# Performance work log

Measured on AMD Instinct MI355X. Metric: run time of the kernel, lower is better.

Reference implementation:

```python
import jax, jax.numpy as jnp
import numpy as np

HEADDIM = 32
BLOCK = 256


def segsum(x):
    """Stable segment sum. x: (..., T) -> (..., T, T) with -inf above diagonal."""
    T = x.shape[-1]
    xe = jnp.broadcast_to(x[..., :, None], x.shape + (T,))  # (..., T, T)
    lower_strict = jnp.tril(jnp.ones((T, T), dtype=bool), -1)
    xe = jnp.where(lower_strict, xe, 0.0)
    x_segsum = jnp.cumsum(xe, axis=-2)
    lower = jnp.tril(jnp.ones((T, T), dtype=bool), 0)
    return jnp.where(lower, x_segsum, -jnp.inf)


def ssd_chunked(X, A, B, C, block_len):
    """Chunked SSD (Mamba2) scan, L assumed divisible by block_len.
    X: (b,L,h,p)  A: (b,L,h)  B,C: (b,L,h,n). Returns Y: (b,L,h,p)."""
    b, L, h, p = X.shape
    c = L // block_len
    X = X.reshape(b, c, block_len, h, p)
    A = A.reshape(b, c, block_len, h).transpose(0, 3, 1, 2)  # b h c l
    B = B.reshape(b, c, block_len, h, -1)
    C = C.reshape(b, c, block_len, h, -1)

    A_cumsum = jnp.cumsum(A, axis=-1)                         # b h c l
    Lmat = jnp.exp(segsum(A))                                 # b h c l s
    Y_diag = jnp.einsum('bclhn,bcshn,bhcls,bcshp->bclhp', C, B, Lmat, X)

    decay_states = jnp.exp(A_cumsum[:, :, :, -1:] - A_cumsum)  # b h c l
    states = jnp.einsum('bclhn,bhcl,bclhp->bchpn', B, decay_states, X)
    init = jnp.zeros_like(states[:, :1])
    states = jnp.concatenate([init, states], axis=1)           # b (c+1) h p n

    chunk_sums = jnp.pad(A_cumsum[:, :, :, -1], ((0, 0), (0, 0), (1, 0)))  # b h (c+1)
    decay_chunk = jnp.exp(segsum(chunk_sums))                  # b h (c+1) (c+1)
    new_states = jnp.einsum('bhzc,bchpn->bzhpn', decay_chunk, states)
    inter_states = new_states[:, :-1]                          # b c h p n

    state_decay_out = jnp.exp(A_cumsum)                        # b h c l
    Y_off = jnp.einsum('bclhn,bchpn,bhcl->bclhp', C, inter_states, state_decay_out)
    return (Y_diag + Y_off).reshape(b, L, h, p)


def setup_inputs() -> dict:
    key = jax.random.key(0)
    k1, k2, k3 = jax.random.split(key, 3)
    Bsz, L, D = 2, 4096, 1024
    hidden_states = jax.random.normal(k1, (Bsz, L, D), dtype=jnp.float32)
    boundary_prob = jax.random.uniform(k2, (Bsz, L), minval=0.01, maxval=0.99, dtype=jnp.float32)
    boundary_mask = jax.random.uniform(k3, (Bsz, L)) < 0.25
    boundary_mask = boundary_mask.at[:, 0].set(True)  # first token must be a boundary
    return {"hidden_states": hidden_states, "boundary_prob": boundary_prob,
            "boundary_mask": boundary_mask}


def reference(hidden_states, boundary_prob, boundary_mask):
    Bsz, L, D = hidden_states.shape
    nheads = D // HEADDIM

    # --- Chunk layer: stable gather of boundary tokens to the front (M = L) ---
    token_idx = jnp.arange(L)[None, :] + (~boundary_mask).astype(jnp.int32) * L
    order = jnp.argsort(token_idx, axis=1)                    # (B, L)
    h = jnp.take_along_axis(hidden_states, order[:, :, None], axis=1)
    p = jnp.take_along_axis(boundary_prob, order, axis=1)

    # --- DeChunk: EMA reconstruction via chunked SSD scan ---
    p = jnp.clip(p, 1e-4, 1.0 - 1e-4)
    dt = jnp.log(1.0 / (1.0 - p))                              # (B, L)
    x = (h / dt[..., None]).reshape(Bsz, L, nheads, HEADDIM)
    X = x * dt[..., None, None]                                # = h, scaled form used by SSD
    A_seq = jnp.broadcast_to(-dt[..., None], (Bsz, L, nheads))  # A = -1 per head
    Bm = jnp.broadcast_to(p[..., None, None], (Bsz, L, nheads, 1))
    Cm = jnp.ones_like(Bm)
    Y = ssd_chunked(X, A_seq, Bm, Cm, BLOCK)                   # (B, L, h, p)
    out = Y.reshape(Bsz, L, D)

    # --- Plug back: each original position reads latest boundary's EMA value ---
    idx = jnp.clip(jnp.cumsum(boundary_mask.astype(jnp.int32), axis=1) - 1, 0, L - 1)
    return jnp.take_along_axis(out, idx[:, :, None], axis=1)
```

## Files before the change

kernel.cpp:

```cpp
#include <hip/hip_runtime.h>
#include <hip/hip_bf16.h>

#define SEQL 4096
#define DIM  1024
#define TR   16
#define LOOKBACK 128
#define WCAP 32
#define DSCUT -8.0f

typedef float f32x4 __attribute__((ext_vector_type(4)));

__global__ __launch_bounds__(256) void solo_kernel(
    const float* __restrict__ h, const float* __restrict__ prob,
    const int* __restrict__ mask, float* __restrict__ out) {
  const int bx  = blockIdx.x;
  const int s   = (bx & 7) * (SEQL / TR / 8) + (bx >> 3);
  const int t0  = s * TR;
  const int b   = blockIdx.y;
  const int tid = threadIdx.x, wid = tid >> 6, lane = tid & 63;
  const int tok = t0 - LOOKBACK + tid;

  __shared__ float lw[WCAP];
  __shared__ int   lp[WCAP];
  __shared__ float inb_b[TR];
  __shared__ int   wsC[4];
  __shared__ float wsS[4];

  int mv = 0; float pv = 0.f, la = 0.f;
  if (tid < LOOKBACK + TR && tok >= 0) {
    mv = (mask[b * SEQL + tok] != 0);
    float p = prob[b * SEQL + tok];
    pv = fminf(fmaxf(p, 1e-4f), 1.f - 1e-4f);
    la = mv ? __logf(1.f - pv) : 0.f;
  }
  if (tid < WCAP) lw[tid] = 0.f;

  int ci = mv; float si = la;
#pragma unroll
  for (int off = 1; off < 64; off <<= 1) {
    int   tc = __shfl_up(ci, off, 64);
    float ts = __shfl_up(si, off, 64);
    if (lane >= off) { ci += tc; si += ts; }
  }
  if (lane == 63) { wsC[wid] = ci; wsS[wid] = si; }
  __syncthreads();

  int woffC = 0, Cref = 0; float woffS = 0.f, Sref = 0.f;
#pragma unroll
  for (int wv = 0; wv < 4; ++wv) {
    int c = wsC[wv]; float s2 = wsS[wv];
    if (wv < wid) { woffC += c; woffS += s2; }
    if (wv < 2)   { Cref  += c; Sref  += s2; }
  }
  const int   C = woffC + ci;
  const float P = woffS + si;

  if (tid < LOOKBACK) {
    if (mv) {
      int idx = Cref - C;
      float dS = Sref - P;
      if (idx < WCAP && dS >= DSCUT) {
        lw[idx] = __expf(dS) * pv;
        lp[idx] = tok;
      }
    }
  } else if (tid < LOOKBACK + TR) {
    inb_b[tid - LOOKBACK] = mv ? pv : 0.f;
  }
  __syncthreads();

  unsigned long long bal = __ballot(lane < WCAP && lw[lane] != 0.f);
  const int wlen = (int)__popcll(bal);

  const float* hb = h + (size_t)b * SEQL * DIM;
  float* ob = out + (size_t)b * SEQL * DIM;
  const int d0 = tid * 4;

  float4 C0 = {0,0,0,0}, C1 = {0,0,0,0}, C2 = {0,0,0,0}, C3 = {0,0,0,0};
  int l = 0;
  for (; l + 4 <= wlen; l += 4) {
    float w0 = lw[l], w1 = lw[l+1], w2 = lw[l+2], w3 = lw[l+3];
    const float4 x0 = *(const float4*)(hb + (size_t)lp[l]   * DIM + d0);
    const float4 x1 = *(const float4*)(hb + (size_t)lp[l+1] * DIM + d0);
    const float4 x2 = *(const float4*)(hb + (size_t)lp[l+2] * DIM + d0);
    const float4 x3 = *(const float4*)(hb + (size_t)lp[l+3] * DIM + d0);
    C0.x = fmaf(w0, x0.x, C0.x); C0.y = fmaf(w0, x0.y, C0.y);
    C0.z = fmaf(w0, x0.z, C0.z); C0.w = fmaf(w0, x0.w, C0.w);
    C1.x = fmaf(w1, x1.x, C1.x); C1.y = fmaf(w1, x1.y, C1.y);
    C1.z = fmaf(w1, x1.z, C1.z); C1.w = fmaf(w1, x1.w, C1.w);
    C2.x = fmaf(w2, x2.x, C2.x); C2.y = fmaf(w2, x2.y, C2.y);
    C2.z = fmaf(w2, x2.z, C2.z); C2.w = fmaf(w2, x2.w, C2.w);
    C3.x = fmaf(w3, x3.x, C3.x); C3.y = fmaf(w3, x3.y, C3.y);
    C3.z = fmaf(w3, x3.z, C3.z); C3.w = fmaf(w3, x3.w, C3.w);
  }
  for (; l < wlen; ++l) {
    float w0 = lw[l];
    const float4 x0 = *(const float4*)(hb + (size_t)lp[l] * DIM + d0);
    C0.x = fmaf(w0, x0.x, C0.x); C0.y = fmaf(w0, x0.y, C0.y);
    C0.z = fmaf(w0, x0.z, C0.z); C0.w = fmaf(w0, x0.w, C0.w);
  }
  f32x4 H;
  H.x = (C0.x + C1.x) + (C2.x + C3.x);
  H.y = (C0.y + C1.y) + (C2.y + C3.y);
  H.z = (C0.z + C1.z) + (C2.z + C3.z);
  H.w = (C0.w + C1.w) + (C2.w + C3.w);

#pragma unroll
  for (int k = 0; k < TR; ++k) {
    float bc = inb_b[k];
    if (bc > 0.f) {
      const float4 x = *(const float4*)(hb + (size_t)(t0 + k) * DIM + d0);
      float a = 1.f - bc;
      H.x = fmaf(a, H.x, bc * x.x);
      H.y = fmaf(a, H.y, bc * x.y);
      H.z = fmaf(a, H.z, bc * x.z);
      H.w = fmaf(a, H.w, bc * x.w);
    }
    __builtin_nontemporal_store(H, (f32x4*)(ob + (size_t)(t0 + k) * DIM + d0));
  }
}

extern "C" void kernel_launch(void* const* d_in, const int* in_sizes, int n_in,
                              void* d_out, int out_size, void* d_ws, size_t ws_size,
                              hipStream_t stream) {
  const float* h    = (const float*)d_in[0];
  const float* p    = (const float*)d_in[1];
  const int*   mask = (const int*)d_in[2];
  float* out = (float*)d_out;

  solo_kernel<<<dim3(SEQL / TR, 2), 256, 0, stream>>>(h, p, mask, out);
}
```

Baseline: 12.97 us.

## Split each 16-row tile across two 256-thread groups with independent lookback windows

Blocks grow to 512 threads. Each 256-thread group handles 8 of the 16 output rows, and each recomputes its own truncated EMA seed from the boundary-token list, so the serial recurrence per thread is halved. Boundary weights are now computed on the fly from stored prefix log-sums, and the tile's own probabilities are read through wave shuffles instead of shared memory. The cost is that the second group repeats the lookback gather, which adds global reads and exp work.

New measurement: 16.34 us. +26.0%, slower.

```diff
diff --git a/kernel.cpp b/kernel.cpp
--- a/kernel.cpp
+++ b/kernel.cpp
@@ -5,12 +5,13 @@
 #define DIM  1024
 #define TR   16
 #define LOOKBACK 128
-#define WCAP 32
+#define NTOK (LOOKBACK + TR)
+#define NSLOT 144
 #define DSCUT -8.0f
 
 typedef float f32x4 __attribute__((ext_vector_type(4)));
 
-__global__ __launch_bounds__(256) void solo_kernel(
+__global__ __launch_bounds__(512, 4) void solo_kernel(
     const float* __restrict__ h, const float* __restrict__ prob,
     const int* __restrict__ mask, float* __restrict__ out) {
   const int bx  = blockIdx.x;
@@ -20,20 +21,28 @@
   const int tid = threadIdx.x, wid = tid >> 6, lane = tid & 63;
   const int tok = t0 - LOOKBACK + tid;
 
-  __shared__ float lw[WCAP];
-  __shared__ int   lp[WCAP];
-  __shared__ float inb_b[TR];
-  __shared__ int   wsC[4];
-  __shared__ float wsS[4];
+  __shared__ int   bTok[NSLOT];
+  __shared__ float bP[NSLOT];
+  __shared__ float bS[NSLOT];
+  __shared__ int   wsC[8];
+  __shared__ float wsS[8];
 
   int mv = 0; float pv = 0.f, la = 0.f;
-  if (tid < LOOKBACK + TR && tok >= 0) {
+  if (tid < NTOK && tok >= 0) {
     mv = (mask[b * SEQL + tok] != 0);
     float p = prob[b * SEQL + tok];
     pv = fminf(fmaxf(p, 1e-4f), 1.f - 1e-4f);
     la = mv ? __logf(1.f - pv) : 0.f;
   }
-  if (tid < WCAP) lw[tid] = 0.f;
+
+  int rmv = 0; float rpv = 0.f, rla = 0.f;
+  if (lane < TR) {
+    rmv = (mask[b * SEQL + t0 + lane] != 0);
+    float p = prob[b * SEQL + t0 + lane];
+    float pc = fminf(fmaxf(p, 1e-4f), 1.f - 1e-4f);
+    rpv = rmv ? pc : 0.f;
+    rla = rmv ? __logf(1.f - pc) : 0.f;
+  }
 
   int ci = mv; float si = la;
 #pragma unroll
@@ -45,78 +54,90 @@
   if (lane == 63) { wsC[wid] = ci; wsS[wid] = si; }
   __syncthreads();
 
-  int woffC = 0, Cref = 0; float woffS = 0.f, Sref = 0.f;
+  int woffC = 0; float woffS = 0.f;
 #pragma unroll
-  for (int wv = 0; wv < 4; ++wv) {
-    int c = wsC[wv]; float s2 = wsS[wv];
-    if (wv < wid) { woffC += c; woffS += s2; }
-    if (wv < 2)   { Cref  += c; Sref  += s2; }
+  for (int wv = 0; wv < 8; ++wv) {
+    if (wv < wid) { woffC += wsC[wv]; woffS += wsS[wv]; }
   }
   const int   C = woffC + ci;
   const float P = woffS + si;
+  const int   Cref1 = wsC[0] + wsC[1];
+  const float Sref1 = wsS[0] + wsS[1];
 
-  if (tid < LOOKBACK) {
-    if (mv) {
-      int idx = Cref - C;
-      float dS = Sref - P;
-      if (idx < WCAP && dS >= DSCUT) {
-        lw[idx] = __expf(dS) * pv;
-        lp[idx] = tok;
-      }
-    }
-  } else if (tid < LOOKBACK + TR) {
-    inb_b[tid - LOOKBACK] = mv ? pv : 0.f;
+  if (tid < NTOK && mv) {
+    int slot = C - 1;
+    bTok[slot] = tok; bP[slot] = pv; bS[slot] = P;
   }
+
+  unsigned long long rbal = __ballot(lane < 8 && rmv);
+  const int nb1 = (int)__popcll(rbal);
+  float Sref2 = Sref1;
+#pragma unroll
+  for (int j = 0; j < 8; ++j) Sref2 += __shfl(rla, j, 64);
   __syncthreads();
 
-  unsigned long long bal = __ballot(lane < WCAP && lw[lane] != 0.f);
-  const int wlen = (int)__popcll(bal);
+  const int grp = tid >> 8;
+  const int gt  = tid & 255;
+  const int d0  = gt * 4;
+  const int r0  = t0 + grp * 8;
+  const float SrefG  = grp ? Sref2 : Sref1;
+  const int   newest = (grp ? Cref1 + nb1 : Cref1) - 1;
+
+  {
+  }
+  int slotL = newest - lane;
+  bool keep = (slotL >= 0) && ((SrefG - bS[slotL]) >= DSCUT);
+  const int wl = (int)__popcll(__ballot(keep));
 
   const float* hb = h + (size_t)b * SEQL * DIM;
   float* ob = out + (size_t)b * SEQL * DIM;
-  const int d0 = tid * 4;
 
-  float4 C0 = {0,0,0,0}, C1 = {0,0,0,0}, C2 = {0,0,0,0}, C3 = {0,0,0,0};
-  int l = 0;
-  for (; l + 4 <= wlen; l += 4) {
-    float w0 = lw[l], w1 = lw[l+1], w2 = lw[l+2], w3 = lw[l+3];
-    const float4 x0 = *(const float4*)(hb + (size_t)lp[l]   * DIM + d0);
-    const float4 x1 = *(const float4*)(hb + (size_t)lp[l+1] * DIM + d0);
-    const float4 x2 = *(const float4*)(hb + (size_t)lp[l+2] * DIM + d0);
-    const float4 x3 = *(const float4*)(hb + (size_t)lp[l+3] * DIM + d0);
-    C0.x = fmaf(w0, x0.x, C0.x); C0.y = fmaf(w0, x0.y, C0.y);
-    C0.z = fmaf(w0, x0.z, C0.z); C0.w = fmaf(w0, x0.w, C0.w);
-    C1.x = fmaf(w1, x1.x, C1.x); C1.y = fmaf(w1, x1.y, C1.y);
-    C1.z = fmaf(w1, x1.z, C1.z); C1.w = fmaf(w1, x1.w, C1.w);
-    C2.x = fmaf(w2, x2.x, C2.x); C2.y = fmaf(w2, x2.y, C2.y);
-    C2.z = fmaf(w2, x2.z, C2.z); C2.w = fmaf(w2, x2.w, C2.w);
-    C3.x = fmaf(w3, x3.x, C3.x); C3.y = fmaf(w3, x3.y, C3.y);
-    C3.z = fmaf(w3, x3.z, C3.z); C3.w = fmaf(w3, x3.w, C3.w);
+  float4 A0 = {0,0,0,0}, A1 = {0,0,0,0}, A2 = {0,0,0,0}, A3 = {0,0,0,0};
+  int r = 0;
+  for (; r + 4 <= wl; r += 4) {
+    int s0 = newest - r, s1 = s0 - 1, s2 = s0 - 2, s3 = s0 - 3;
+    float w0 = __expf(SrefG - bS[s0]) * bP[s0];
+    float w1 = __expf(SrefG - bS[s1]) * bP[s1];
+    float w2 = __expf(SrefG - bS[s2]) * bP[s2];
+    float w3 = __expf(SrefG - bS[s3]) * bP[s3];
+    const float4 x0 = *(const float4*)(hb + (size_t)bTok[s0] * DIM + d0);
+    const float4 x1 = *(const float4*)(hb + (size_t)bTok[s1] * DIM + d0);
+    const float4 x2 = *(const float4*)(hb + (size_t)bTok[s2] * DIM + d0);
+    const float4 x3 = *(const float4*)(hb + (size_t)bTok[s3] * DIM + d0);
+    A0.x = fmaf(w0, x0.x, A0.x); A0.y = fmaf(w0, x0.y, A0.y);
+    A0.z = fmaf(w0, x0.z, A0.z); A0.w = fmaf(w0, x0.w, A0.w);
+    A1.x = fmaf(w1, x1.x, A1.x); A1.y = fmaf(w1, x1.y, A1.y);
+    A1.z = fmaf(w1, x1.z, A1.z); A1.w = fmaf(w1, x1.w, A1.w);
+    A2.x = fmaf(w2, x2.x, A2.x); A2.y = fmaf(w2, x2.y, A2.y);
+    A2.z = fmaf(w2, x2.z, A2.z); A2.w = fmaf(w2, x2.w, A2.w);
+    A3.x = fmaf(w3, x3.x, A3.x); A3.y = fmaf(w3, x3.y, A3.y);
+    A3.z = fmaf(w3, x3.z, A3.z); A3.w = fmaf(w3, x3.w, A3.w);
   }
-  for (; l < wlen; ++l) {
-    float w0 = lw[l];
-    const float4 x0 = *(const float4*)(hb + (size_t)lp[l] * DIM + d0);
-    C0.x = fmaf(w0, x0.x, C0.x); C0.y = fmaf(w0, x0.y, C0.y);
-    C0.z = fmaf(w0, x0.z, C0.z); C0.w = fmaf(w0, x0.w, C0.w);
+  for (; r < wl; ++r) {
+    int s0 = newest - r;
+    float w0 = __expf(SrefG - bS[s0]) * bP[s0];
+    const float4 x0 = *(const float4*)(hb + (size_t)bTok[s0] * DIM + d0);
+    A0.x = fmaf(w0, x0.x, A0.x); A0.y = fmaf(w0, x0.y, A0.y);
+    A0.z = fmaf(w0, x0.z, A0.z); A0.w = fmaf(w0, x0.w, A0.w);
   }
   f32x4 H;
-  H.x = (C0.x + C1.x) + (C2.x + C3.x);
-  H.y = (C0.y + C1.y) + (C2.y + C3.y);
-  H.z = (C0.z + C1.z) + (C2.z + C3.z);
-  H.w = (C0.w + C1.w) + (C2.w + C3.w);
+  H.x = (A0.x + A1.x) + (A2.x + A3.x);
+  H.y = (A0.y + A1.y) + (A2.y + A3.y);
+  H.z = (A0.z + A1.z) + (A2.z + A3.z);
+  H.w = (A0.w + A1.w) + (A2.w + A3.w);
 
 #pragma unroll
-  for (int k = 0; k < TR; ++k) {
-    float bc = inb_b[k];
+  for (int k = 0; k < 8; ++k) {
+    float bc = __shfl(rpv, grp * 8 + k, 64);
     if (bc > 0.f) {
-      const float4 x = *(const float4*)(hb + (size_t)(t0 + k) * DIM + d0);
+      const float4 x = *(const float4*)(hb + (size_t)(r0 + k) * DIM + d0);
       float a = 1.f - bc;
       H.x = fmaf(a, H.x, bc * x.x);
       H.y = fmaf(a, H.y, bc * x.y);
       H.z = fmaf(a, H.z, bc * x.z);
       H.w = fmaf(a, H.w, bc * x.w);
     }
-    __builtin_nontemporal_store(H, (f32x4*)(ob + (size_t)(t0 + k) * DIM + d0));
+    __builtin_nontemporal_store(H, (f32x4*)(ob + (size_t)(r0 + k) * DIM + d0));
   }
 }
 
@@ -128,5 +149,5 @@
   const int*   mask = (const int*)d_in[2];
   float* out = (float*)d_out;
 
-  solo_kernel<<<dim3(SEQL / TR, 2), 256, 0, stream>>>(h, p, mask, out);
+  solo_kernel<<<dim3(SEQL / TR, 2), 512, 0, stream>>>(h, p, mask, out);
 }
```
